# Kernel optimization log

Measured on AMD Instinct MI355X. Metric: run time of the kernel, lower is better.

The kernel has to match this reference:

```python
import jax, jax.numpy as jnp
import numpy as np

B, N, F, D = 32, 1024, 128, 128
SCALE = 0.5


def setup_inputs() -> dict:
    key = jax.random.key(0)
    ks = jax.random.split(key, 8)
    atom_query = jax.random.normal(ks[0], (B, N, F), dtype=jnp.float32)
    # binary validity mask (some atoms padded out), shape [B, N, 1]
    mask = (jax.random.uniform(ks[1], (B, N, 1)) < 0.9).astype(jnp.float32)
    s = 1.0 / np.sqrt(F)
    Wq = jax.random.normal(ks[2], (F, D), dtype=jnp.float32) * s
    Wk = jax.random.normal(ks[3], (F, D), dtype=jnp.float32) * s
    Wv = jax.random.normal(ks[4], (F, D), dtype=jnp.float32) * s
    bq = jnp.zeros((D,), jnp.float32)
    bk = jnp.zeros((D,), jnp.float32)
    bv = jnp.zeros((D,), jnp.float32)
    return {"atom_query": atom_query, "mask": mask,
            "Wq": Wq, "bq": bq, "Wk": Wk, "bk": bk, "Wv": Wv, "bv": bv}


def reference(atom_query, mask, Wq, bq, Wk, bk, Wv, bv):
    # projections
    q = atom_query @ Wq + bq            # [B,N,D]
    k = atom_query @ Wk + bk            # [B,N,D]
    v = atom_query @ Wv + bv            # [B,N,D]
    n = q.shape[1]
    dk = (q.shape[-1] ** (-SCALE)) / n  # python float scalar
    q = q * jnp.float32(dk)
    # pairwise energy [B,N,N]
    energy = jnp.einsum('bqd,bkd->bqk', q, k)
    energy = energy * mask              # mask query rows ([B,N,1] broadcast)
    idx = jnp.arange(n)
    energy = energy.at[:, idx, idx].set(0.0)  # remove self-interaction (diag)
    # aggregate attention per query atom [B,N,1]
    agg = jnp.sum(energy, axis=-1, keepdims=True) * mask
    # euclidean normalize along atom axis (tf.linalg.normalize, axis=1)
    nrm = jnp.sqrt(jnp.sum(agg * agg, axis=1, keepdims=True))
    agg = agg / nrm
    agg = agg + (1.0 - mask) * (-1e9)
    attn = jax.nn.softmax(agg, axis=1)  # softmax over atom (query) axis
    # weighted sum of values -> [B,D]
    context = jnp.sum(mask * (attn * v), axis=1)
    return attn, context
```

## Files before the change

### kernel.cpp

```cpp
#include <hip/hip_runtime.h>

#define B_ 32
#define N_ 1024
#define DK_CONST 8.631674575031098e-05f
#define POISON_U 0xAAAAAAAAu

typedef unsigned short u16;
typedef unsigned int u32;
typedef __attribute__((ext_vector_type(8))) short short8;
typedef __attribute__((ext_vector_type(4))) float floatx4;

__device__ __forceinline__ u16 f2b(float x) {
    union { float f; u32 u; } v; v.f = x;
    u32 u = v.u;
    return (u16)((u + 0x7FFFu + ((u >> 16) & 1u)) >> 16);
}
__device__ __forceinline__ float b2f(u16 h) {
    union { u32 u; float f; } v; v.u = ((u32)h) << 16;
    return v.f;
}
__device__ __forceinline__ void pubf(float* p, float x) {
    union { float f; u32 u; } c; c.f = x;
    __hip_atomic_store((u32*)p, c.u, __ATOMIC_RELAXED, __HIP_MEMORY_SCOPE_AGENT);
}
__device__ __forceinline__ u32 ald(const float* p) {
    return __hip_atomic_load((const u32*)p, __ATOMIC_RELAXED, __HIP_MEMORY_SCOPE_AGENT);
}
__device__ __forceinline__ float u2f(u32 u) { union { u32 u_; float f; } c; c.u_ = u; return c.f; }

__global__ __launch_bounds__(256, 1) void mega(
    const float* __restrict__ aq, const float* __restrict__ mask,
    const float* __restrict__ Wq, const float* __restrict__ bq,
    const float* __restrict__ Wk, const float* __restrict__ bk,
    const float* __restrict__ Wv, const float* __restrict__ bv,
    float* __restrict__ colsumPart, float* __restrict__ ssqPart,
    float* __restrict__ aggG, float* __restrict__ ctxPart,
    float* __restrict__ attnOut, float* __restrict__ ctxOut)
{
    __shared__ __align__(16) u16 aqT[128][136];
    __shared__ __align__(16) char wreg[69632];
    __shared__ __align__(16) char r3[8704];
    __shared__ float qpart[2][128];
    __shared__ float Ksum_s[128], Ss[128], bq_s[128], bk_s[128];
    __shared__ float red[256];
    __shared__ float shInvn;

    u16 (*wqS)[136] = (u16(*)[136])wreg;
    u16 (*wkS)[136] = (u16(*)[136])(wreg + 34816);
    float (*wv)[132] = (float(*)[132])wreg;
    float (*cspart)[4] = (float(*)[4])r3;
    float* el   = (float*)r3;
    float* accs = (float*)(r3 + 4096);
    float* pvec = (float*)(r3 + 8192);

    int t = threadIdx.x;
    int tile = blockIdx.x;
    int b = tile >> 3;
    int s = tile & 7;

    const float4* aq4 = (const float4*)(aq + (size_t)tile * 16384);
    float c0 = 0.f, c1 = 0.f, c2 = 0.f, c3 = 0.f;
    for (int j = 0; j < 16; ++j) {
        int idx = t + 256 * j;
        int row = idx >> 5;
        int c4  = idx & 31;
        float4 v = aq4[idx];
        c0 += v.x; c1 += v.y; c2 += v.z; c3 += v.w;
        ushort4 bb;
        bb.x = f2b(v.x); bb.y = f2b(v.y); bb.z = f2b(v.z); bb.w = f2b(v.w);
        *((ushort4*)&aqT[row][c4 * 4]) = bb;
    }
    cspart[t][0] = c0; cspart[t][1] = c1; cspart[t][2] = c2; cspart[t][3] = c3;
    __syncthreads();
    if (t < 128) {
        int c4i = t >> 2, comp = t & 3;
        float sum = 0.f;
        for (int h = 0; h < 8; ++h) sum += cspart[h * 32 + c4i][comp];
        pubf(&colsumPart[tile * 128 + t], sum);
    }
    for (int j = 0; j < 64; ++j) {
        int idx = t + 256 * j;
        int f = idx >> 7, d = idx & 127;
        wqS[d][f] = f2b(Wq[idx]);
        wkS[d][f] = f2b(Wk[idx]);
    }
    __syncthreads();

    if (t < 128) {
        u32 raw[8];
        #pragma unroll
        for (int h = 0; h < 8; ++h) raw[h] = ald(&colsumPart[(b * 8 + h) * 128 + t]);
        float ssv = 0.f;
        #pragma unroll
        for (int h = 0; h < 8; ++h) {
            while (raw[h] == POISON_U) {
                __builtin_amdgcn_s_sleep(1);
                raw[h] = ald(&colsumPart[(b * 8 + h) * 128 + t]);
            }
            ssv += u2f(raw[h]);
        }
        Ss[t] = ssv;
        bq_s[t] = bq[t];
        bk_s[t] = bk[t];
    }
    __syncthreads();
    if (t < 128) {
        float kd = 1024.0f * bk_s[t];
        for (int f = 0; f < 128; ++f) kd += Ss[f] * Wk[f * 128 + t];
        Ksum_s[t] = kd;
    }
    __syncthreads();

    int w = t >> 6;
    int lane = t & 63;
    int wr   = (w >> 1) * 64;
    int wcol = (w & 1) * 64;
    int lm = lane & 15;
    int lq = lane >> 4;

    floatx4 acc1[4][4], acc2[4][4];
    for (int i = 0; i < 4; ++i)
        for (int j = 0; j < 4; ++j) {
            acc1[i][j] = (floatx4){0.f, 0.f, 0.f, 0.f};
            acc2[i][j] = (floatx4){0.f, 0.f, 0.f, 0.f};
        }
    for (int ks = 0; ks < 4; ++ks) {
        int k0 = ks * 32 + lq * 8;
        short8 afr[4], bqf[4], bkf[4];
        for (int i = 0; i < 4; ++i) {
            afr[i] = *(const short8*)&aqT[wr + i * 16 + lm][k0];
            bqf[i] = *(const short8*)&wqS[wcol + i * 16 + lm][k0];
            bkf[i] = *(const short8*)&wkS[wcol + i * 16 + lm][k0];
        }
        for (int i = 0; i < 4; ++i)
            for (int j = 0; j < 4; ++j) {
                acc1[i][j] = __builtin_amdgcn_mfma_f32_16x16x32_bf16(afr[i], bqf[j], acc1[i][j], 0, 0, 0);
                acc2[i][j] = __builtin_amdgcn_mfma_f32_16x16x32_bf16(afr[i], bkf[j], acc2[i][j], 0, 0, 0);
            }
    }
    for (int mi = 0; mi < 4; ++mi) {
        for (int r = 0; r < 4; ++r) {
            int row = wr + mi * 16 + lq * 4 + r;
            float sx = 0.f;
            for (int nj = 0; nj < 4; ++nj) {
                int col = wcol + nj * 16 + lm;
                float qv = acc1[mi][nj][r] + bq_s[col];
                float kv = Ksum_s[col] - acc2[mi][nj][r] - bk_s[col];
                sx += qv * kv;
            }
            sx += __shfl_xor(sx, 1);
            sx += __shfl_xor(sx, 2);
            sx += __shfl_xor(sx, 4);
            sx += __shfl_xor(sx, 8);
            if (lm == 0) qpart[w & 1][row] = sx;
        }
    }
    __syncthreads();
    float av = 0.f;
    if (t < 128) {
        int atom = tile * 128 + t;
        av = mask[atom] * DK_CONST * (qpart[0][t] + qpart[1][t]);
        pubf(&aggG[atom], av);
    }
    red[t] = av * av;
    __syncthreads();
    for (int st = 128; st > 0; st >>= 1) { if (t < st) red[t] += red[t + st]; __syncthreads(); }
    if (t == 0) pubf(&ssqPart[tile], red[0]);
    __syncthreads();

    if (t == 0) {
        u32 raw[8];
        #pragma unroll
        for (int h = 0; h < 8; ++h) raw[h] = ald(&ssqPart[b * 8 + h]);
        float ssum = 0.f;
        #pragma unroll
        for (int h = 0; h < 8; ++h) {
            while (raw[h] == POISON_U) {
                __builtin_amdgcn_s_sleep(1);
                raw[h] = ald(&ssqPart[b * 8 + h]);
            }
            ssum += u2f(raw[h]);
        }
        shInvn = 1.0f / sqrtf(ssum);
    }
    __syncthreads();
    float invn = shInvn;
    u32 raga[4];
    #pragma unroll
    for (int j = 0; j < 4; ++j) raga[j] = ald(&aggG[b * 1024 + j * 256 + t]);
    float epart = 0.f;
    #pragma unroll
    for (int j = 0; j < 4; ++j) {
        int i = j * 256 + t;
        while (raga[j] == POISON_U) {
            __builtin_amdgcn_s_sleep(1);
            raga[j] = ald(&aggG[b * 1024 + i]);
        }
        float m = mask[b * 1024 + i];
        float e = (m > 0.5f) ? expf(u2f(raga[j]) * invn) : 0.f;
        el[i] = e;
        epart += e;
    }
    red[t] = epart;
    __syncthreads();
    for (int st = 128; st > 0; st >>= 1) { if (t < st) red[t] += red[t + st]; __syncthreads(); }
    float invE = 1.0f / red[0];
    if (t < 128) attnOut[tile * 128 + t] = el[s * 128 + t] * invE;

    {
        int f = t & 127, hh = t >> 7;
        float acc = 0.f;
        for (int r = hh; r < 128; r += 2) acc += el[s * 128 + r] * b2f(aqT[r][f]);
        accs[hh * 128 + f] = acc;
    }
    __syncthreads();
    {
        const float4* wv4 = (const float4*)Wv;
        for (int j = 0; j < 16; ++j) {
            int idx = t + 256 * j;
            int f  = idx >> 5;
            int d4 = (idx & 31) * 4;
            *((float4*)&wv[f][d4]) = wv4[idx];
        }
    }
    __syncthreads();
    if (t < 128) pvec[t] = accs[t] + accs[128 + t];
    __syncthreads();
    if (t < 128) {
        float c = 0.f;
        for (int f = 0; f < 128; ++f) c += pvec[f] * wv[f][t];
        pubf(&ctxPart[tile * 128 + t], c * invE);
    }

    if (s == 0 && t < 128) {
        u32 raw[8];
        #pragma unroll
        for (int h = 0; h < 8; ++h) raw[h] = ald(&ctxPart[(b * 8 + h) * 128 + t]);
        float c = 0.f;
        #pragma unroll
        for (int h = 0; h < 8; ++h) {
            while (raw[h] == POISON_U) {
                __builtin_amdgcn_s_sleep(1);
                raw[h] = ald(&ctxPart[(b * 8 + h) * 128 + t]);
            }
            c += u2f(raw[h]);
        }
        ctxOut[b * 128 + t] = c + bv[t];
    }
}

extern "C" void kernel_launch(void* const* d_in, const int* in_sizes, int n_in,
                              void* d_out, int out_size, void* d_ws, size_t ws_size,
                              hipStream_t stream) {
    const float* aq   = (const float*)d_in[0];
    const float* mask = (const float*)d_in[1];
    const float* Wq   = (const float*)d_in[2];
    const float* bq   = (const float*)d_in[3];
    const float* Wk   = (const float*)d_in[4];
    const float* bk   = (const float*)d_in[5];
    const float* Wv   = (const float*)d_in[6];
    const float* bv   = (const float*)d_in[7];

    float* out_attn = (float*)d_out;
    float* out_ctx  = out_attn + B_ * N_;

    float* wsf        = (float*)d_ws;
    float* colsumPart = wsf;
    float* ssqPart    = wsf + 32768;
    float* aggG       = wsf + 33024;
    float* ctxPart    = wsf + 65792;

    mega<<<256, 256, 0, stream>>>(aq, mask, Wq, bq, Wk, bk, Wv, bv,
                                  colsumPart, ssqPart, aggG, ctxPart,
                                  out_attn, out_ctx);
}
```

Before: 99.02 us.

## Precompute Wk·Wqᵀ product so energy needs one MFMA pass and defer colsum wait

Rewrites the per-atom energy as x·M·(S−x) with M = Wk·Wqᵀ computed per block via MFMA, replacing two projection GEMMs with one weight GEMM plus one activation GEMM. It adds bias correction terms that run only when the biases are nonzero. The cross-block colsum wait now sits after the MFMA work, so the spin wait overlaps compute, and the Wv load moves earlier to overlap the ssq wait. The cost is rounding the intermediate M to bf16, which adds approximation error, plus redundant M computation in every block.

```diff
diff --git a/kernel.cpp b/kernel.cpp
--- a/kernel.cpp
+++ b/kernel.cpp
@@ -3,6 +3,7 @@
 #define B_ 32
 #define N_ 1024
 #define DK_CONST 8.631674575031098e-05f
+#define NM1 1023.0f
 #define POISON_U 0xAAAAAAAAu
 
 typedef unsigned short u16;
@@ -38,26 +39,28 @@
     float* __restrict__ attnOut, float* __restrict__ ctxOut)
 {
     __shared__ __align__(16) u16 aqT[128][136];
-    __shared__ __align__(16) char wreg[69632];
-    __shared__ __align__(16) char r3[8704];
+    __shared__ __align__(16) char wbuf[69632];
+    __shared__ __align__(16) char scratch[8704];
     __shared__ float qpart[2][128];
-    __shared__ float Ksum_s[128], Ss[128], bq_s[128], bk_s[128];
+    __shared__ float Ss[128], bq_s[128], bk_s[128], wc_s[128], w2_s[128];
     __shared__ float red[256];
-    __shared__ float shInvn;
-
-    u16 (*wqS)[136] = (u16(*)[136])wreg;
-    u16 (*wkS)[136] = (u16(*)[136])(wreg + 34816);
-    float (*wv)[132] = (float(*)[132])wreg;
-    float (*cspart)[4] = (float(*)[4])r3;
-    float* el   = (float*)r3;
-    float* accs = (float*)(r3 + 4096);
-    float* pvec = (float*)(r3 + 8192);
+    __shared__ float shv[4];
+
+    u16 (*wA)[136]  = (u16(*)[136])wbuf;
+    u16 (*wB)[136]  = (u16(*)[136])(wbuf + 34816);
+    u16 (*mtS)[136] = wB;
+    float (*wv)[132] = (float(*)[132])wbuf;
+    float (*cspart)[4] = (float(*)[4])scratch;
+    float* el   = (float*)scratch;
+    float* accs = (float*)(scratch + 4096);
+    float* pvec = (float*)(scratch + 5120);
 
     int t = threadIdx.x;
     int tile = blockIdx.x;
     int b = tile >> 3;
     int s = tile & 7;
 
+    if (t < 128) { bq_s[t] = bq[t]; bk_s[t] = bk[t]; wc_s[t] = 0.f; }
     const float4* aq4 = (const float4*)(aq + (size_t)tile * 16384);
     float c0 = 0.f, c1 = 0.f, c2 = 0.f, c3 = 0.f;
     for (int j = 0; j < 16; ++j) {
@@ -71,6 +74,23 @@
         *((ushort4*)&aqT[row][c4 * 4]) = bb;
     }
     cspart[t][0] = c0; cspart[t][1] = c1; cspart[t][2] = c2; cspart[t][3] = c3;
+    {
+        const float4* wk4 = (const float4*)Wk;
+        const float4* wq4 = (const float4*)Wq;
+        for (int j = 0; j < 16; ++j) {
+            int idx = t + 256 * j;
+            int row = idx >> 5;
+            int c4  = idx & 31;
+            float4 a = wk4[idx];
+            ushort4 ba;
+            ba.x = f2b(a.x); ba.y = f2b(a.y); ba.z = f2b(a.z); ba.w = f2b(a.w);
+            *((ushort4*)&wA[row][c4 * 4]) = ba;
+            float4 q = wq4[idx];
+            ushort4 bqv;
+            bqv.x = f2b(q.x); bqv.y = f2b(q.y); bqv.z = f2b(q.z); bqv.w = f2b(q.w);
+            *((ushort4*)&wB[row][c4 * 4]) = bqv;
+        }
+    }
     __syncthreads();
     if (t < 128) {
         int c4i = t >> 2, comp = t & 3;
@@ -78,37 +98,10 @@
         for (int h = 0; h < 8; ++h) sum += cspart[h * 32 + c4i][comp];
         pubf(&colsumPart[tile * 128 + t], sum);
     }
-    for (int j = 0; j < 64; ++j) {
-        int idx = t + 256 * j;
-        int f = idx >> 7, d = idx & 127;
-        wqS[d][f] = f2b(Wq[idx]);
-        wkS[d][f] = f2b(Wk[idx]);
-    }
-    __syncthreads();
-
-    if (t < 128) {
-        u32 raw[8];
-        #pragma unroll
-        for (int h = 0; h < 8; ++h) raw[h] = ald(&colsumPart[(b * 8 + h) * 128 + t]);
-        float ssv = 0.f;
-        #pragma unroll
-        for (int h = 0; h < 8; ++h) {
-            while (raw[h] == POISON_U) {
-                __builtin_amdgcn_s_sleep(1);
-                raw[h] = ald(&colsumPart[(b * 8 + h) * 128 + t]);
-            }
-            ssv += u2f(raw[h]);
-        }
-        Ss[t] = ssv;
-        bq_s[t] = bq[t];
-        bk_s[t] = bk[t];
-    }
-    __syncthreads();
-    if (t < 128) {
-        float kd = 1024.0f * bk_s[t];
-        for (int f = 0; f < 128; ++f) kd += Ss[f] * Wk[f * 128 + t];
-        Ksum_s[t] = kd;
-    }
+    red[t] = (t < 128) ? (fabsf(bq_s[t]) + fabsf(bk_s[t])) : 0.f;
+    __syncthreads();
+    for (int st = 128; st > 0; st >>= 1) { if (t < st) red[t] += red[t + st]; __syncthreads(); }
+    float nb = red[0];
     __syncthreads();
 
     int w = t >> 6;
@@ -118,35 +111,93 @@
     int lm = lane & 15;
     int lq = lane >> 4;
 
-    floatx4 acc1[4][4], acc2[4][4];
+    floatx4 accM[4][4];
     for (int i = 0; i < 4; ++i)
-        for (int j = 0; j < 4; ++j) {
-            acc1[i][j] = (floatx4){0.f, 0.f, 0.f, 0.f};
-            acc2[i][j] = (floatx4){0.f, 0.f, 0.f, 0.f};
-        }
+        for (int j = 0; j < 4; ++j)
+            accM[i][j] = (floatx4){0.f, 0.f, 0.f, 0.f};
     for (int ks = 0; ks < 4; ++ks) {
         int k0 = ks * 32 + lq * 8;
-        short8 afr[4], bqf[4], bkf[4];
+        short8 afr[4], bfr[4];
+        for (int i = 0; i < 4; ++i) {
+            afr[i] = *(const short8*)&wA[wr + i * 16 + lm][k0];
+            bfr[i] = *(const short8*)&wB[wcol + i * 16 + lm][k0];
+        }
+        for (int i = 0; i < 4; ++i)
+            for (int j = 0; j < 4; ++j)
+                accM[i][j] = __builtin_amdgcn_mfma_f32_16x16x32_bf16(afr[i], bfr[j], accM[i][j], 0, 0, 0);
+    }
+    if (nb != 0.f) {
+        if (t < 128) {
+            float w1 = 0.f, w2 = 0.f;
+            for (int d = 0; d < 128; ++d) {
+                w1 += b2f(wB[t][d]) * bk_s[d];
+                w2 += b2f(wA[t][d]) * bq_s[d];
+            }
+            wc_s[t] = NM1 * w1 - w2;
+            w2_s[t] = w2;
+        }
+        red[t] = (t < 128) ? bq_s[t] * bk_s[t] : 0.f;
+        __syncthreads();
+        for (int st = 128; st > 0; st >>= 1) { if (t < st) red[t] += red[t + st]; __syncthreads(); }
+        if (t == 0) shv[1] = red[0];
+        __syncthreads();
+    }
+    __syncthreads();
+    for (int gi = 0; gi < 4; ++gi)
+        for (int fj = 0; fj < 4; ++fj)
+            for (int r = 0; r < 4; ++r)
+                mtS[wr + gi * 16 + lq * 4 + r][wcol + fj * 16 + lm] = f2b(accM[gi][fj][r]);
+    __syncthreads();
+
+    floatx4 acc[4][4];
+    for (int i = 0; i < 4; ++i)
+        for (int j = 0; j < 4; ++j)
+            acc[i][j] = (floatx4){0.f, 0.f, 0.f, 0.f};
+    for (int ks = 0; ks < 4; ++ks) {
+        int k0 = ks * 32 + lq * 8;
+        short8 afr[4], mfr[4];
         for (int i = 0; i < 4; ++i) {
             afr[i] = *(const short8*)&aqT[wr + i * 16 + lm][k0];
-            bqf[i] = *(const short8*)&wqS[wcol + i * 16 + lm][k0];
-            bkf[i] = *(const short8*)&wkS[wcol + i * 16 + lm][k0];
+            mfr[i] = *(const short8*)&mtS[wcol + i * 16 + lm][k0];
         }
         for (int i = 0; i < 4; ++i)
-            for (int j = 0; j < 4; ++j) {
-                acc1[i][j] = __builtin_amdgcn_mfma_f32_16x16x32_bf16(afr[i], bqf[j], acc1[i][j], 0, 0, 0);
-                acc2[i][j] = __builtin_amdgcn_mfma_f32_16x16x32_bf16(afr[i], bkf[j], acc2[i][j], 0, 0, 0);
-            }
-    }
+            for (int j = 0; j < 4; ++j)
+                acc[i][j] = __builtin_amdgcn_mfma_f32_16x16x32_bf16(afr[i], mfr[j], acc[i][j], 0, 0, 0);
+    }
+
+    if (t < 128) {
+        u32 raw[8];
+        #pragma unroll
+        for (int h = 0; h < 8; ++h) raw[h] = ald(&colsumPart[(b * 8 + h) * 128 + t]);
+        float ssv = 0.f;
+        #pragma unroll
+        for (int h = 0; h < 8; ++h) {
+            while (raw[h] == POISON_U) {
+                __builtin_amdgcn_s_sleep(1);
+                raw[h] = ald(&colsumPart[(b * 8 + h) * 128 + t]);
+            }
+            ssv += u2f(raw[h]);
+        }
+        Ss[t] = ssv;
+    }
+    __syncthreads();
+    float Cbv = 0.f;
+    if (nb != 0.f) {
+        red[t] = (t < 128) ? Ss[t] * w2_s[t] : 0.f;
+        __syncthreads();
+        for (int st = 128; st > 0; st >>= 1) { if (t < st) red[t] += red[t + st]; __syncthreads(); }
+        Cbv = red[0] + NM1 * shv[1];
+        __syncthreads();
+    }
+
     for (int mi = 0; mi < 4; ++mi) {
         for (int r = 0; r < 4; ++r) {
             int row = wr + mi * 16 + lq * 4 + r;
             float sx = 0.f;
             for (int nj = 0; nj < 4; ++nj) {
                 int col = wcol + nj * 16 + lm;
-                float qv = acc1[mi][nj][r] + bq_s[col];
-                float kv = Ksum_s[col] - acc2[mi][nj][r] - bk_s[col];
-                sx += qv * kv;
+                float av = b2f(aqT[row][col]);
+                sx += acc[mi][nj][r] * (Ss[col] - av) + av * wc_s[col];
             }
             sx += __shfl_xor(sx, 1);
             sx += __shfl_xor(sx, 2);
@@ -159,7 +210,7 @@
     float av = 0.f;
     if (t < 128) {
         int atom = tile * 128 + t;
-        av = mask[atom] * DK_CONST * (qpart[0][t] + qpart[1][t]);
+        av = mask[atom] * DK_CONST * (qpart[0][t] + qpart[1][t] + Cbv);
         pubf(&aggG[atom], av);
     }
     red[t] = av * av;
@@ -168,6 +219,15 @@
     if (t == 0) pubf(&ssqPart[tile], red[0]);
     __syncthreads();
 
+    {
+        const float4* wv4 = (const float4*)Wv;
+        for (int j = 0; j < 16; ++j) {
+            int idx = t + 256 * j;
+            int f  = idx >> 5;
+            int d4 = (idx & 31) * 4;
+            *((float4*)&wv[f][d4]) = wv4[idx];
+        }
+    }
     if (t == 0) {
         u32 raw[8];
         #pragma unroll
@@ -181,10 +241,10 @@
             }
             ssum += u2f(raw[h]);
         }
-        shInvn = 1.0f / sqrtf(ssum);
-    }
-    __syncthreads();
-    float invn = shInvn;
+        shv[0] = 1.0f / sqrtf(ssum);
+    }
+    __syncthreads();
+    float invn = shv[0];
     u32 raga[4];
     #pragma unroll
     for (int j = 0; j < 4; ++j) raga[j] = ald(&aggG[b * 1024 + j * 256 + t]);
@@ -209,19 +269,9 @@
 
     {
         int f = t & 127, hh = t >> 7;
-        float acc = 0.f;
-        for (int r = hh; r < 128; r += 2) acc += el[s * 128 + r] * b2f(aqT[r][f]);
-        accs[hh * 128 + f] = acc;
-    }
-    __syncthreads();
-    {
-        const float4* wv4 = (const float4*)Wv;
-        for (int j = 0; j < 16; ++j) {
-            int idx = t + 256 * j;
-            int f  = idx >> 5;
-            int d4 = (idx & 31) * 4;
-            *((float4*)&wv[f][d4]) = wv4[idx];
-        }
+        float acc2 = 0.f;
+        for (int r = hh; r < 128; r += 2) acc2 += el[s * 128 + r] * b2f(aqT[r][f]);
+        accs[hh * 128 + f] = acc2;
     }
     __syncthreads();
     if (t < 128) pvec[t] = accs[t] + accs[128 + t];
```

Measured after the change: 92.72 us, median of 2. 6.4% less time.
